# Kernel tuning notes

Hardware: AMD Instinct MI355X
Metric: run time of the kernel (lower is better)

## Reference

```python
import jax, jax.numpy as jnp
import numpy as np

LN_EPS = 1e-5

def _ln(x, g, b):
    # LayerNorm over last dim; torch normalized_shape=[1,H] on [B,1,H] reduces to this
    mu = jnp.mean(x, axis=-1, keepdims=True)
    var = jnp.var(x, axis=-1, keepdims=True)
    return (x - mu) * jax.lax.rsqrt(var + LN_EPS) * g + b


def setup_inputs() -> dict:
    key = jax.random.key(0)
    B, T, D, H = 32, 2048, 512, 128
    ks = jax.random.split(key, 10)
    stdu = 1.0 / np.sqrt(H)
    u = lambda k, sh: jax.random.uniform(k, sh, jnp.float32, -stdu, stdu)
    return {
        "x": jax.random.normal(ks[0], (B, T, D), jnp.float32),
        "W_f": u(ks[1], (D, H)), "W_i": u(ks[2], (D, H)),
        "W_o": u(ks[3], (D, H)), "W_c": u(ks[4], (D, H)),
        "U_f": u(ks[5], (H, H)), "U_i": u(ks[6], (H, H)),
        "U_o": u(ks[7], (H, H)), "U_c": u(ks[8], (H, H)),
        "b_f": jnp.ones((H,), jnp.float32),
        "b_i": jnp.zeros((H,), jnp.float32),
        "b_o": jnp.zeros((H,), jnp.float32),
        "b_c": jnp.zeros((H,), jnp.float32),
        "ln_f_g": jnp.ones((H,), jnp.float32), "ln_f_b": jnp.zeros((H,), jnp.float32),
        "ln_i_g": jnp.ones((H,), jnp.float32), "ln_i_b": jnp.zeros((H,), jnp.float32),
        "ln_o_g": jnp.ones((H,), jnp.float32), "ln_o_b": jnp.zeros((H,), jnp.float32),
        "ln_c_g": jnp.ones((H,), jnp.float32), "ln_c_b": jnp.zeros((H,), jnp.float32),
        "h0": jnp.zeros((B, H), jnp.float32),
        "c0": jnp.zeros((B, H), jnp.float32),
        "zoneout_mask": jax.random.randint(ks[9], (T,), 0, 2, jnp.int32),
    }


def reference(x, W_f, W_i, W_o, W_c, U_f, U_i, U_o, U_c,
              b_f, b_i, b_o, b_c,
              ln_f_g, ln_f_b, ln_i_g, ln_i_b, ln_o_g, ln_o_b, ln_c_g, ln_c_b,
              h0, c0, zoneout_mask):
    xs = jnp.swapaxes(x, 0, 1)                       # [T, B, D]
    m = zoneout_mask.astype(x.dtype)[:, None, None]  # [T, 1, 1] zoneout indicator

    def step(carry, inp):
        h, c = carry
        x_t, mt = inp
        f = jax.nn.sigmoid(_ln(x_t @ W_f + h @ U_f + b_f, ln_f_g, ln_f_b))
        i = jax.nn.sigmoid(_ln(x_t @ W_i + h @ U_i + b_i, ln_i_g, ln_i_b))
        o = jax.nn.sigmoid(_ln(x_t @ W_o + h @ U_o + b_o, ln_o_g, ln_o_b))
        ch = jax.nn.sigmoid(_ln(x_t @ W_c + h @ U_c + b_c, ln_c_g, ln_c_b))
        c_new = mt * c + (1.0 - mt) * (f * c + i * ch)
        # NOTE: source applies sigmoid (not tanh) to the cell state
        h_new = mt * h + (1.0 - mt) * (o * jax.nn.sigmoid(c_new))
        return (h_new, c_new), h_new

    (h_T, c_T), out_seq = jax.lax.scan(step, (h0, c0), (xs, m))
    return jnp.swapaxes(out_seq, 0, 1), h_T          # [B, T, H], [B, H]
```

## Files before the change

### kernel.cpp

```cpp
#include <hip/hip_runtime.h>
#include <hip/hip_bf16.h>

#define Bx 32
#define Tt 2048
#define Dd 512
#define Hh 128
#define PROW 520

typedef __attribute__((ext_vector_type(8))) short short8;
typedef __attribute__((ext_vector_type(4))) float f32x4;

static __device__ __forceinline__ short f2bf(float f) {
    __hip_bfloat16 h = __float2bfloat16(f);
    return *reinterpret_cast<short*>(&h);
}
static __device__ __forceinline__ float sigm(float x) {
    return 1.f / (1.f + __expf(-x));
}
static __device__ __forceinline__ float swz_xor16(float v) {
    return __int_as_float(__builtin_amdgcn_ds_swizzle(__float_as_int(v), 0x401F));
}

#define BARRIER_LGKM() asm volatile("s_waitcnt lgkmcnt(0)\n\ts_barrier" ::: "memory")

typedef __attribute__((address_space(1))) const void gas_void;
typedef __attribute__((address_space(3))) void las_void;
static __device__ __forceinline__ void gl_lds16(const float* g, float* l) {
    __builtin_amdgcn_global_load_lds((gas_void*)g, (las_void*)l, 16, 0, 0);
}

__global__ __launch_bounds__(512, 2) void gemm_xw_mfma(
    const float* __restrict__ X,
    const float* __restrict__ W0, const float* __restrict__ W1,
    const float* __restrict__ W2, const float* __restrict__ W3,
    const float* __restrict__ B0, const float* __restrict__ B1,
    const float* __restrict__ B2, const float* __restrict__ B3,
    float* __restrict__ G)
{
    __shared__ __align__(16) short As[128][40];
    __shared__ __align__(16) short Bs[512][40];

    const int tid  = threadIdx.x;
    const int m0   = blockIdx.x * 128;
    const int lane = tid & 63;
    const int w    = tid >> 6;
    const int wr   = w >> 2, wc = w & 3;
    const int l15  = lane & 15, kb = lane >> 4;

    const int bn   = tid;
    const int gate = bn >> 7;
    const int j    = bn & 127;
    const float* __restrict__ Wg = (gate == 0) ? W0 : (gate == 1) ? W1 : (gate == 2) ? W2 : W3;

    const int am = tid >> 2;
    const int ak = (tid & 3) * 8;

    const float* __restrict__ Bg = (wc == 0) ? B0 : (wc == 1) ? B1 : (wc == 2) ? B2 : B3;
    f32x4 acc[4][8];
    #pragma unroll
    for (int nt = 0; nt < 8; ++nt) {
        const float bv = Bg[nt * 16 + l15];
        #pragma unroll
        for (int mt = 0; mt < 4; ++mt)
            acc[mt][nt] = (f32x4){bv, bv, bv, bv};
    }

    for (int k0 = 0; k0 < Dd; k0 += 32) {
        {
            const float4* xp = (const float4*)&X[(size_t)(m0 + am) * Dd + k0 + ak];
            float4 v0 = xp[0], v1 = xp[1];
            short8 s;
            s[0] = f2bf(v0.x); s[1] = f2bf(v0.y); s[2] = f2bf(v0.z); s[3] = f2bf(v0.w);
            s[4] = f2bf(v1.x); s[5] = f2bf(v1.y); s[6] = f2bf(v1.z); s[7] = f2bf(v1.w);
            *(short8*)&As[am][ak] = s;
        }
        #pragma unroll
        for (int rc = 0; rc < 4; ++rc) {
            float v[8];
            #pragma unroll
            for (int r = 0; r < 8; ++r)
                v[r] = Wg[(size_t)(k0 + rc * 8 + r) * Hh + j];
            short8 s;
            #pragma unroll
            for (int r = 0; r < 8; ++r) s[r] = f2bf(v[r]);
            *(short8*)&Bs[bn][rc * 8] = s;
        }
        __syncthreads();

        short8 a[4], b[8];
        #pragma unroll
        for (int mt = 0; mt < 4; ++mt)
            a[mt] = *(const short8*)&As[wr * 64 + mt * 16 + l15][kb * 8];
        #pragma unroll
        for (int nt = 0; nt < 8; ++nt)
            b[nt] = *(const short8*)&Bs[wc * 128 + nt * 16 + l15][kb * 8];
        #pragma unroll
        for (int mt = 0; mt < 4; ++mt)
            #pragma unroll
            for (int nt = 0; nt < 8; ++nt)
                acc[mt][nt] = __builtin_amdgcn_mfma_f32_16x16x32_bf16(a[mt], b[nt], acc[mt][nt], 0, 0, 0);
        __syncthreads();
    }

    #pragma unroll
    for (int mt = 0; mt < 4; ++mt)
        #pragma unroll
        for (int nt = 0; nt < 8; ++nt)
            #pragma unroll
            for (int r = 0; r < 4; ++r)
                G[(size_t)(m0 + wr * 64 + mt * 16 + kb * 4 + r) * 512 + wc * 128 + nt * 16 + l15]
                    = acc[mt][nt][r];
}

__global__ __launch_bounds__(512, 1) void lstm_scan_mfma(
    const float* __restrict__ G,
    const float* __restrict__ Uf, const float* __restrict__ Ui,
    const float* __restrict__ Uo, const float* __restrict__ Uc,
    const float* __restrict__ lnfg, const float* __restrict__ lnfb,
    const float* __restrict__ lnig, const float* __restrict__ lnib,
    const float* __restrict__ lnog, const float* __restrict__ lnob,
    const float* __restrict__ lncg, const float* __restrict__ lncb,
    const float* __restrict__ h0, const float* __restrict__ c0,
    const int* __restrict__ zmask,
    float* __restrict__ out, float* __restrict__ hT)
{
    const int tid  = threadIdx.x;
    const int lane = tid & 63;
    const int w    = tid >> 6;
    const int b0   = blockIdx.x * 4;

    __shared__ __align__(16) short Ap[16 * 136];
    __shared__ __align__(16) float STb[4 * PROW];
    __shared__ __align__(16) float2 SQf[4][4][2][2];
    __shared__ __align__(16) float Pan[2 * 4 * 4 * PROW];
    __shared__ unsigned short act[Tt];
    __shared__ int wsum[8], wpre[8];
    __shared__ int nact_sh;

    const int gate = w >> 1;
    const float* __restrict__ Ug = (gate == 0) ? Uf : (gate == 1) ? Ui : (gate == 2) ? Uo : Uc;
    const int n0  = w * 64;
    const int l15 = lane & 15;
    const int kb  = lane >> 4;

    short8 bfr[4][4];
    #pragma unroll
    for (int nt = 0; nt < 4; ++nt) {
        const int jloc = (n0 & 127) + nt * 16 + l15;
        #pragma unroll
        for (int ks = 0; ks < 4; ++ks) {
            short8 v;
            #pragma unroll
            for (int r = 0; r < 8; ++r)
                v[r] = f2bf(Ug[(ks * 32 + kb * 8 + r) * Hh + jloc]);
            bfr[nt][ks] = v;
        }
    }

    const int ob = tid >> 7;
    const int oj = tid & 127;
    const float gamF = lnfg[oj], betF = lnfb[oj];
    const float gamI = lnig[oj], betI = lnib[oj];
    const float gamO = lnog[oj], betO = lnob[oj];
    const float gamC = lncg[oj], betC = lncb[oj];

    float hval = h0[(b0 + ob) * Hh + oj];
    float cval = c0[(b0 + ob) * Hh + oj];

    for (int i = tid; i < 16 * 136; i += 512) Ap[i] = 0;
    __syncthreads();
    Ap[ob * 136 + oj] = f2bf(hval);

    {
        const int base_t = tid * 4;
        const int f0 = (zmask[base_t] == 0), f1 = (zmask[base_t + 1] == 0);
        const int f2 = (zmask[base_t + 2] == 0), f3 = (zmask[base_t + 3] == 0);
        const int cnt = f0 + f1 + f2 + f3;
        int scan = cnt;
        #pragma unroll
        for (int off = 1; off <= 32; off <<= 1) {
            int v = __shfl_up(scan, off);
            if (lane >= off) scan += v;
        }
        if (lane == 63) wsum[w] = scan;
        __syncthreads();
        if (tid == 0) {
            int s = 0;
            #pragma unroll
            for (int i = 0; i < 8; ++i) { wpre[i] = s; s += wsum[i]; }
            nact_sh = s;
        }
        __syncthreads();
        int pos = wpre[w] + scan - cnt;
        if (f0) act[pos++] = (unsigned short)(base_t);
        if (f1) act[pos++] = (unsigned short)(base_t + 1);
        if (f2) act[pos++] = (unsigned short)(base_t + 2);
        if (f3) act[pos++] = (unsigned short)(base_t + 3);
    }
    __syncthreads();
    const int nact = nact_sh;

    auto stage_panel = [&](int kp, int buf) {
        #pragma unroll
        for (int si = 0; si < 2; ++si) {
            const int s    = w * 2 + si;
            const int slot = s >> 2;
            const int bb   = s & 3;
            const int kidx = kp + slot;
            if (kidx < nact) {
                const int tt = (int)act[kidx];
                const float* src = &G[((size_t)(b0 + bb) * Tt + tt) * 512];
                float* dst = &Pan[((buf * 4 + slot) * 4 + bb) * PROW];
                gl_lds16(src + lane * 4, dst);
                gl_lds16(src + 256 + lane * 4, dst + 256);
            }
        }
    };

    int cur = 0;
    stage_panel(0, 0);
    asm volatile("s_waitcnt vmcnt(0)" ::: "memory");
    __syncthreads();

    const int lb = l15 & 3;

    auto lstm_step = [&](int kidx, int slot) {
        const int t_ = (int)act[kidx];

        short8 a0 = *(const short8*)&Ap[l15 * 136 +  0 + kb * 8];
        short8 a1 = *(const short8*)&Ap[l15 * 136 + 32 + kb * 8];
        short8 a2 = *(const short8*)&Ap[l15 * 136 + 64 + kb * 8];
        short8 a3 = *(const short8*)&Ap[l15 * 136 + 96 + kb * 8];

        const int pbase = ((cur * 4 + slot) * 4 + lb) * PROW + n0 + kb * 4;
        f32x4 C0 = *(const f32x4*)&Pan[pbase];
        f32x4 C1 = *(const f32x4*)&Pan[pbase + 16];
        f32x4 C2 = *(const f32x4*)&Pan[pbase + 32];
        f32x4 C3 = *(const f32x4*)&Pan[pbase + 48];

        C0 = __builtin_amdgcn_mfma_f32_16x16x32_bf16(bfr[0][0], a0, C0, 0, 0, 0);
        C1 = __builtin_amdgcn_mfma_f32_16x16x32_bf16(bfr[1][0], a0, C1, 0, 0, 0);
        C2 = __builtin_amdgcn_mfma_f32_16x16x32_bf16(bfr[2][0], a0, C2, 0, 0, 0);
        C3 = __builtin_amdgcn_mfma_f32_16x16x32_bf16(bfr[3][0], a0, C3, 0, 0, 0);
        C0 = __builtin_amdgcn_mfma_f32_16x16x32_bf16(bfr[0][1], a1, C0, 0, 0, 0);
        C1 = __builtin_amdgcn_mfma_f32_16x16x32_bf16(bfr[1][1], a1, C1, 0, 0, 0);
        C2 = __builtin_amdgcn_mfma_f32_16x16x32_bf16(bfr[2][1], a1, C2, 0, 0, 0);
        C3 = __builtin_amdgcn_mfma_f32_16x16x32_bf16(bfr[3][1], a1, C3, 0, 0, 0);
        C0 = __builtin_amdgcn_mfma_f32_16x16x32_bf16(bfr[0][2], a2, C0, 0, 0, 0);
        C1 = __builtin_amdgcn_mfma_f32_16x16x32_bf16(bfr[1][2], a2, C1, 0, 0, 0);
        C2 = __builtin_amdgcn_mfma_f32_16x16x32_bf16(bfr[2][2], a2, C2, 0, 0, 0);
        C3 = __builtin_amdgcn_mfma_f32_16x16x32_bf16(bfr[3][2], a2, C3, 0, 0, 0);
        C0 = __builtin_amdgcn_mfma_f32_16x16x32_bf16(bfr[0][3], a3, C0, 0, 0, 0);
        C1 = __builtin_amdgcn_mfma_f32_16x16x32_bf16(bfr[1][3], a3, C1, 0, 0, 0);
        C2 = __builtin_amdgcn_mfma_f32_16x16x32_bf16(bfr[2][3], a3, C2, 0, 0, 0);
        C3 = __builtin_amdgcn_mfma_f32_16x16x32_bf16(bfr[3][3], a3, C3, 0, 0, 0);

        float ps = ((C0[0] + C0[1]) + (C0[2] + C0[3]))
                 + ((C1[0] + C1[1]) + (C1[2] + C1[3]))
                 + ((C2[0] + C2[1]) + (C2[2] + C2[3]))
                 + ((C3[0] + C3[1]) + (C3[2] + C3[3]));
        float pq = C0[0]*C0[0] + C0[1]*C0[1] + C0[2]*C0[2] + C0[3]*C0[3]
                 + C1[0]*C1[0] + C1[1]*C1[1] + C1[2]*C1[2] + C1[3]*C1[3]
                 + C2[0]*C2[0] + C2[1]*C2[1] + C2[2]*C2[2] + C2[3]*C2[3]
                 + C3[0]*C3[0] + C3[1]*C3[1] + C3[2]*C3[2] + C3[3]*C3[3];
        ps += swz_xor16(ps);
        pq += swz_xor16(pq);

        if (l15 < 4) {
            const int sbase = l15 * PROW + n0 + kb * 4;
            *(f32x4*)&STb[sbase]      = C0;
            *(f32x4*)&STb[sbase + 16] = C1;
            *(f32x4*)&STb[sbase + 32] = C2;
            *(f32x4*)&STb[sbase + 48] = C3;
            if ((kb & 1) == 0)
                SQf[gate][l15][w & 1][kb >> 1] = make_float2(ps, pq);
        }
        BARRIER_LGKM();

        const float sF = STb[ob * PROW +   0 + oj];
        const float sI = STb[ob * PROW + 128 + oj];
        const float sO = STb[ob * PROW + 256 + oj];
        const float sC = STb[ob * PROW + 384 + oj];
        f32x4 qF0 = *(const f32x4*)&SQf[0][ob][0][0];
        f32x4 qF1 = *(const f32x4*)&SQf[0][ob][1][0];
        f32x4 qI0 = *(const f32x4*)&SQf[1][ob][0][0];
        f32x4 qI1 = *(const f32x4*)&SQf[1][ob][1][0];
        f32x4 qO0 = *(const f32x4*)&SQf[2][ob][0][0];
        f32x4 qO1 = *(const f32x4*)&SQf[2][ob][1][0];
        f32x4 qC0 = *(const f32x4*)&SQf[3][ob][0][0];
        f32x4 qC1 = *(const f32x4*)&SQf[3][ob][1][0];
        const float SF = (qF0[0] + qF0[2]) + (qF1[0] + qF1[2]);
        const float QF = (qF0[1] + qF0[3]) + (qF1[1] + qF1[3]);
        const float SI = (qI0[0] + qI0[2]) + (qI1[0] + qI1[2]);
        const float QI = (qI0[1] + qI0[3]) + (qI1[1] + qI1[3]);
        const float SO = (qO0[0] + qO0[2]) + (qO1[0] + qO1[2]);
        const float QO = (qO0[1] + qO0[3]) + (qO1[1] + qO1[3]);
        const float SC = (qC0[0] + qC0[2]) + (qC1[0] + qC1[2]);
        const float QC = (qC0[1] + qC0[3]) + (qC1[1] + qC1[3]);
        const float muF = SF * (1.f/128.f), rF = rsqrtf(QF*(1.f/128.f) - muF*muF + 1e-5f);
        const float muI = SI * (1.f/128.f), rI = rsqrtf(QI*(1.f/128.f) - muI*muI + 1e-5f);
        const float muO = SO * (1.f/128.f), rO = rsqrtf(QO*(1.f/128.f) - muO*muO + 1e-5f);
        const float muC = SC * (1.f/128.f), rC = rsqrtf(QC*(1.f/128.f) - muC*muC + 1e-5f);
        const float gf  = sigm((sF - muF) * rF * gamF + betF);
        const float gi  = sigm((sI - muI) * rI * gamI + betI);
        const float go  = sigm((sO - muO) * rO * gamO + betO);
        const float gch = sigm((sC - muC) * rC * gamC + betC);
        cval = gf * cval + gi * gch;
        hval = go * sigm(cval);
        Ap[ob * 136 + oj] = f2bf(hval);
        out[((size_t)(b0 + ob) * Tt + t_) * Hh + oj] = hval;
    };

    for (int kp = 0; kp < nact; kp += 4) {
        stage_panel(kp + 4, cur ^ 1);
        const int lim = (nact - kp < 4) ? (nact - kp) : 4;
        #pragma unroll
        for (int sl = 0; sl < 4; ++sl) {
            if (sl < lim) {
                lstm_step(kp + sl, sl);
                if (sl == 3)
                    asm volatile("s_waitcnt vmcnt(0)" ::: "memory");
                BARRIER_LGKM();
            }
        }
        cur ^= 1;
    }

    hT[(b0 + ob) * Hh + oj] = hval;
}

__global__ __launch_bounds__(512) void fill_zoneout(
    const int* __restrict__ zmask, const float* __restrict__ h0,
    float* __restrict__ out)
{
    const int t = blockIdx.x;
    if (zmask[t] == 0) return;
    int s = t - 1;
    while (s >= 0 && zmask[s] != 0) --s;
    const int tid = threadIdx.x;
    for (int idx = tid; idx < Bx * Hh; idx += 512) {
        const int b = idx >> 7, j = idx & 127;
        const float v = (s >= 0) ? out[((size_t)b * Tt + s) * Hh + j]
                                 : h0[b * Hh + j];
        out[((size_t)b * Tt + t) * Hh + j] = v;
    }
}

extern "C" void kernel_launch(void* const* d_in, const int* in_sizes, int n_in,
                              void* d_out, int out_size, void* d_ws, size_t ws_size,
                              hipStream_t stream)
{
    const float* x   = (const float*)d_in[0];
    const float* W_f = (const float*)d_in[1];
    const float* W_i = (const float*)d_in[2];
    const float* W_o = (const float*)d_in[3];
    const float* W_c = (const float*)d_in[4];
    const float* U_f = (const float*)d_in[5];
    const float* U_i = (const float*)d_in[6];
    const float* U_o = (const float*)d_in[7];
    const float* U_c = (const float*)d_in[8];
    const float* b_f = (const float*)d_in[9];
    const float* b_i = (const float*)d_in[10];
    const float* b_o = (const float*)d_in[11];
    const float* b_c = (const float*)d_in[12];
    const float* ln_f_g = (const float*)d_in[13];
    const float* ln_f_b = (const float*)d_in[14];
    const float* ln_i_g = (const float*)d_in[15];
    const float* ln_i_b = (const float*)d_in[16];
    const float* ln_o_g = (const float*)d_in[17];
    const float* ln_o_b = (const float*)d_in[18];
    const float* ln_c_g = (const float*)d_in[19];
    const float* ln_c_b = (const float*)d_in[20];
    const float* h0  = (const float*)d_in[21];
    const float* c0  = (const float*)d_in[22];
    const int*   zm  = (const int*)d_in[23];

    float* out = (float*)d_out;
    float* hT  = out + (size_t)Bx * Tt * Hh;
    float* G   = (float*)d_ws;

    gemm_xw_mfma<<<(Bx * Tt) / 128, 512, 0, stream>>>(x, W_f, W_i, W_o, W_c,
                                                      b_f, b_i, b_o, b_c, G);

    lstm_scan_mfma<<<8, 512, 0, stream>>>(G, U_f, U_i, U_o, U_c,
                                          ln_f_g, ln_f_b, ln_i_g, ln_i_b,
                                          ln_o_g, ln_o_b, ln_c_g, ln_c_b,
                                          h0, c0, zm, out, hT);

    fill_zoneout<<<Tt, 512, 0, stream>>>(zm, h0, out);
}
```

Baseline: 1.738 ms.

## Remap scan waves to own all four gates per hidden slice, keeping activations in registers

Each wave now computes all four gate pre-activations for a 16-column slice of the hidden dimension, instead of one gate over 64 columns. The gate nonlinearity and cell update can then run directly on the MFMA accumulators in registers, with no round trip through a shared staging buffer. LayerNorm statistics are reduced through small partial-sum arrays and a single-wave DPP reduction, at the cost of an extra barrier per timestep. The elementwise stage now runs only in the 4-of-16 lanes that hold valid batch rows, so it uses fewer threads, but each does more work with vectorized stores.

Result: slower. 2.687 ms (+54.6%).

```diff
diff --git a/kernel.cpp b/kernel.cpp
--- a/kernel.cpp
+++ b/kernel.cpp
@@ -17,8 +17,10 @@
 static __device__ __forceinline__ float sigm(float x) {
     return 1.f / (1.f + __expf(-x));
 }
-static __device__ __forceinline__ float swz_xor16(float v) {
-    return __int_as_float(__builtin_amdgcn_ds_swizzle(__float_as_int(v), 0x401F));
+template<int CTRL>
+static __device__ __forceinline__ float dpp_add(float v) {
+    return v + __int_as_float(__builtin_amdgcn_update_dpp(
+        0, __float_as_int(v), CTRL, 0xF, 0xF, true));
 }
 
 #define BARRIER_LGKM() asm volatile("s_waitcnt lgkmcnt(0)\n\ts_barrier" ::: "memory")
@@ -129,47 +131,52 @@
     const int w    = tid >> 6;
     const int b0   = blockIdx.x * 4;
 
+    const int l15 = lane & 15;
+    const int kb  = lane >> 4;
+    const int lb  = l15 & 3;
+    const int j0  = w * 16;
+    const int jj  = j0 + kb * 4;
+
     __shared__ __align__(16) short Ap[16 * 136];
-    __shared__ __align__(16) float STb[4 * PROW];
-    __shared__ __align__(16) float2 SQf[4][4][2][2];
+    __shared__ __align__(16) float partPS[4 * 132];
+    __shared__ __align__(16) float partPQ[4 * 132];
+    __shared__ __align__(16) float2 stats[16];
     __shared__ __align__(16) float Pan[2 * 4 * 4 * PROW];
     __shared__ unsigned short act[Tt];
     __shared__ int wsum[8], wpre[8];
     __shared__ int nact_sh;
 
-    const int gate = w >> 1;
-    const float* __restrict__ Ug = (gate == 0) ? Uf : (gate == 1) ? Ui : (gate == 2) ? Uo : Uc;
-    const int n0  = w * 64;
-    const int l15 = lane & 15;
-    const int kb  = lane >> 4;
-
     short8 bfr[4][4];
     #pragma unroll
-    for (int nt = 0; nt < 4; ++nt) {
-        const int jloc = (n0 & 127) + nt * 16 + l15;
+    for (int g = 0; g < 4; ++g) {
+        const float* __restrict__ Ug = (g == 0) ? Uf : (g == 1) ? Ui : (g == 2) ? Uo : Uc;
         #pragma unroll
         for (int ks = 0; ks < 4; ++ks) {
             short8 v;
             #pragma unroll
             for (int r = 0; r < 8; ++r)
-                v[r] = f2bf(Ug[(ks * 32 + kb * 8 + r) * Hh + jloc]);
-            bfr[nt][ks] = v;
-        }
-    }
-
-    const int ob = tid >> 7;
-    const int oj = tid & 127;
-    const float gamF = lnfg[oj], betF = lnfb[oj];
-    const float gamI = lnig[oj], betI = lnib[oj];
-    const float gamO = lnog[oj], betO = lnob[oj];
-    const float gamC = lncg[oj], betC = lncb[oj];
-
-    float hval = h0[(b0 + ob) * Hh + oj];
-    float cval = c0[(b0 + ob) * Hh + oj];
+                v[r] = f2bf(Ug[(ks * 32 + kb * 8 + r) * Hh + j0 + l15]);
+            bfr[g][ks] = v;
+        }
+    }
+
+    f32x4 gam[4], bet[4];
+    gam[0] = *(const f32x4*)&lnfg[jj]; bet[0] = *(const f32x4*)&lnfb[jj];
+    gam[1] = *(const f32x4*)&lnig[jj]; bet[1] = *(const f32x4*)&lnib[jj];
+    gam[2] = *(const f32x4*)&lnog[jj]; bet[2] = *(const f32x4*)&lnob[jj];
+    gam[3] = *(const f32x4*)&lncg[jj]; bet[3] = *(const f32x4*)&lncb[jj];
+
+    f32x4 cv = *(const f32x4*)&c0[(b0 + lb) * Hh + jj];
+    f32x4 hv = *(const f32x4*)&h0[(b0 + lb) * Hh + jj];
 
     for (int i = tid; i < 16 * 136; i += 512) Ap[i] = 0;
     __syncthreads();
-    Ap[ob * 136 + oj] = f2bf(hval);
+    if (l15 < 4) {
+        short hp[4];
+        #pragma unroll
+        for (int r = 0; r < 4; ++r) hp[r] = f2bf(hv[r]);
+        *(short4*)&Ap[l15 * 136 + jj] = *(short4*)hp;
+    }
 
     {
         const int base_t = tid * 4;
@@ -222,8 +229,6 @@
     asm volatile("s_waitcnt vmcnt(0)" ::: "memory");
     __syncthreads();
 
-    const int lb = l15 & 3;
-
     auto lstm_step = [&](int kidx, int slot) {
         const int t_ = (int)act[kidx];
 
@@ -232,11 +237,11 @@
         short8 a2 = *(const short8*)&Ap[l15 * 136 + 64 + kb * 8];
         short8 a3 = *(const short8*)&Ap[l15 * 136 + 96 + kb * 8];
 
-        const int pbase = ((cur * 4 + slot) * 4 + lb) * PROW + n0 + kb * 4;
-        f32x4 C0 = *(const f32x4*)&Pan[pbase];
-        f32x4 C1 = *(const f32x4*)&Pan[pbase + 16];
-        f32x4 C2 = *(const f32x4*)&Pan[pbase + 32];
-        f32x4 C3 = *(const f32x4*)&Pan[pbase + 48];
+        const int pbase = ((cur * 4 + slot) * 4 + lb) * PROW;
+        f32x4 C0 = *(const f32x4*)&Pan[pbase +   0 + jj];
+        f32x4 C1 = *(const f32x4*)&Pan[pbase + 128 + jj];
+        f32x4 C2 = *(const f32x4*)&Pan[pbase + 256 + jj];
+        f32x4 C3 = *(const f32x4*)&Pan[pbase + 384 + jj];
 
         C0 = __builtin_amdgcn_mfma_f32_16x16x32_bf16(bfr[0][0], a0, C0, 0, 0, 0);
         C1 = __builtin_amdgcn_mfma_f32_16x16x32_bf16(bfr[1][0], a0, C1, 0, 0, 0);
@@ -255,60 +260,64 @@
         C2 = __builtin_amdgcn_mfma_f32_16x16x32_bf16(bfr[2][3], a3, C2, 0, 0, 0);
         C3 = __builtin_amdgcn_mfma_f32_16x16x32_bf16(bfr[3][3], a3, C3, 0, 0, 0);
 
-        float ps = ((C0[0] + C0[1]) + (C0[2] + C0[3]))
-                 + ((C1[0] + C1[1]) + (C1[2] + C1[3]))
-                 + ((C2[0] + C2[1]) + (C2[2] + C2[3]))
-                 + ((C3[0] + C3[1]) + (C3[2] + C3[3]));
-        float pq = C0[0]*C0[0] + C0[1]*C0[1] + C0[2]*C0[2] + C0[3]*C0[3]
-                 + C1[0]*C1[0] + C1[1]*C1[1] + C1[2]*C1[2] + C1[3]*C1[3]
-                 + C2[0]*C2[0] + C2[1]*C2[1] + C2[2]*C2[2] + C2[3]*C2[3]
-                 + C3[0]*C3[0] + C3[1]*C3[1] + C3[2]*C3[2] + C3[3]*C3[3];
-        ps += swz_xor16(ps);
-        pq += swz_xor16(pq);
-
+        f32x4 psv, pqv;
+        psv[0] = (C0[0] + C0[1]) + (C0[2] + C0[3]);
+        psv[1] = (C1[0] + C1[1]) + (C1[2] + C1[3]);
+        psv[2] = (C2[0] + C2[1]) + (C2[2] + C2[3]);
+        psv[3] = (C3[0] + C3[1]) + (C3[2] + C3[3]);
+        pqv[0] = C0[0]*C0[0] + C0[1]*C0[1] + C0[2]*C0[2] + C0[3]*C0[3];
+        pqv[1] = C1[0]*C1[0] + C1[1]*C1[1] + C1[2]*C1[2] + C1[3]*C1[3];
+        pqv[2] = C2[0]*C2[0] + C2[1]*C2[1] + C2[2]*C2[2] + C2[3]*C2[3];
+        pqv[3] = C3[0]*C3[0] + C3[1]*C3[1] + C3[2]*C3[2] + C3[3]*C3[3];
         if (l15 < 4) {
-            const int sbase = l15 * PROW + n0 + kb * 4;
-            *(f32x4*)&STb[sbase]      = C0;
-            *(f32x4*)&STb[sbase + 16] = C1;
-            *(f32x4*)&STb[sbase + 32] = C2;
-            *(f32x4*)&STb[sbase + 48] = C3;
-            if ((kb & 1) == 0)
-                SQf[gate][l15][w & 1][kb >> 1] = make_float2(ps, pq);
+            const int pa = l15 * 132 + (w * 4 + kb) * 4;
+            *(f32x4*)&partPS[pa] = psv;
+            *(f32x4*)&partPQ[pa] = pqv;
         }
         BARRIER_LGKM();
 
-        const float sF = STb[ob * PROW +   0 + oj];
-        const float sI = STb[ob * PROW + 128 + oj];
-        const float sO = STb[ob * PROW + 256 + oj];
-        const float sC = STb[ob * PROW + 384 + oj];
-        f32x4 qF0 = *(const f32x4*)&SQf[0][ob][0][0];
-        f32x4 qF1 = *(const f32x4*)&SQf[0][ob][1][0];
-        f32x4 qI0 = *(const f32x4*)&SQf[1][ob][0][0];
-        f32x4 qI1 = *(const f32x4*)&SQf[1][ob][1][0];
-        f32x4 qO0 = *(const f32x4*)&SQf[2][ob][0][0];
-        f32x4 qO1 = *(const f32x4*)&SQf[2][ob][1][0];
-        f32x4 qC0 = *(const f32x4*)&SQf[3][ob][0][0];
-        f32x4 qC1 = *(const f32x4*)&SQf[3][ob][1][0];
-        const float SF = (qF0[0] + qF0[2]) + (qF1[0] + qF1[2]);
-        const float QF = (qF0[1] + qF0[3]) + (qF1[1] + qF1[3]);
-        const float SI = (qI0[0] + qI0[2]) + (qI1[0] + qI1[2]);
-        const float QI = (qI0[1] + qI0[3]) + (qI1[1] + qI1[3]);
-        const float SO = (qO0[0] + qO0[2]) + (qO1[0] + qO1[2]);
-        const float QO = (qO0[1] + qO0[3]) + (qO1[1] + qO1[3]);
-        const float SC = (qC0[0] + qC0[2]) + (qC1[0] + qC1[2]);
-        const float QC = (qC0[1] + qC0[3]) + (qC1[1] + qC1[3]);
-        const float muF = SF * (1.f/128.f), rF = rsqrtf(QF*(1.f/128.f) - muF*muF + 1e-5f);
-        const float muI = SI * (1.f/128.f), rI = rsqrtf(QI*(1.f/128.f) - muI*muI + 1e-5f);
-        const float muO = SO * (1.f/128.f), rO = rsqrtf(QO*(1.f/128.f) - muO*muO + 1e-5f);
-        const float muC = SC * (1.f/128.f), rC = rsqrtf(QC*(1.f/128.f) - muC*muC + 1e-5f);
-        const float gf  = sigm((sF - muF) * rF * gamF + betF);
-        const float gi  = sigm((sI - muI) * rI * gamI + betI);
-        const float go  = sigm((sO - muO) * rO * gamO + betO);
-        const float gch = sigm((sC - muC) * rC * gamC + betC);
-        cval = gf * cval + gi * gch;
-        hval = go * sigm(cval);
-        Ap[ob * 136 + oj] = f2bf(hval);
-        out[((size_t)(b0 + ob) * Tt + t_) * Hh + oj] = hval;
+        if (w == 0) {
+            const int bg = lane >> 2;
+            const int bq = bg >> 2, gq = bg & 3;
+            const int ch = lane & 3;
+            float S = 0.f, Q = 0.f;
+            #pragma unroll
+            for (int i = 0; i < 8; ++i) {
+                const int pa = bq * 132 + (ch * 8 + i) * 4 + gq;
+                S += partPS[pa];
+                Q += partPQ[pa];
+            }
+            S = dpp_add<0xB1>(S); S = dpp_add<0x4E>(S);
+            Q = dpp_add<0xB1>(Q); Q = dpp_add<0x4E>(Q);
+            if (ch == 0) stats[bg] = make_float2(S, Q);
+        }
+        BARRIER_LGKM();
+
+        if (l15 < 4) {
+            f32x4 st01 = *(const f32x4*)&stats[l15 * 4];
+            f32x4 st23 = *(const f32x4*)&stats[l15 * 4 + 2];
+            const float mu0 = st01[0] * (1.f/128.f), r0 = rsqrtf(st01[1]*(1.f/128.f) - mu0*mu0 + 1e-5f);
+            const float mu1 = st01[2] * (1.f/128.f), r1 = rsqrtf(st01[3]*(1.f/128.f) - mu1*mu1 + 1e-5f);
+            const float mu2 = st23[0] * (1.f/128.f), r2 = rsqrtf(st23[1]*(1.f/128.f) - mu2*mu2 + 1e-5f);
+            const float mu3 = st23[2] * (1.f/128.f), r3 = rsqrtf(st23[3]*(1.f/128.f) - mu3*mu3 + 1e-5f);
+            f32x4 hnew;
+            #pragma unroll
+            for (int r = 0; r < 4; ++r) {
+                const float gf  = sigm((C0[r] - mu0) * r0 * gam[0][r] + bet[0][r]);
+                const float gi  = sigm((C1[r] - mu1) * r1 * gam[1][r] + bet[1][r]);
+                const float go  = sigm((C2[r] - mu2) * r2 * gam[2][r] + bet[2][r]);
+                const float gch = sigm((C3[r] - mu3) * r3 * gam[3][r] + bet[3][r]);
+                cv[r] = gf * cv[r] + gi * gch;
+                hnew[r] = go * sigm(cv[r]);
+            }
+            hv = hnew;
+            short hp[4];
+            #pragma unroll
+            for (int r = 0; r < 4; ++r) hp[r] = f2bf(hv[r]);
+            *(short4*)&Ap[l15 * 136 + jj] = *(short4*)hp;
+            float4 ho = make_float4(hv[0], hv[1], hv[2], hv[3]);
+            *(float4*)&out[((size_t)(b0 + l15) * Tt + t_) * Hh + jj] = ho;
+        }
     };
 
     for (int kp = 0; kp < nact; kp += 4) {
@@ -326,7 +335,10 @@
         cur ^= 1;
     }
 
-    hT[(b0 + ob) * Hh + oj] = hval;
+    if (l15 < 4) {
+        float4 ho = make_float4(hv[0], hv[1], hv[2], hv[3]);
+        *(float4*)&hT[(b0 + l15) * Hh + jj] = ho;
+    }
 }
 
 __global__ __launch_bounds__(512) void fill_zoneout(
```

## Assign one wave per gate in LSTM scan to keep LayerNorm stats in-wave

Applied to the files above, without the earlier changes.

The recurrent scan kernel drops from 8 waves to 4, and each wave now computes the full 128-wide pre-activation for one gate. LayerNorm mean and variance are therefore reduced entirely within the wave using a swizzle plus a shuffle, and each wave normalises its own values before writing them to shared memory. This removes the cross-wave exchange of partial statistics and simplifies the gate epilogue. In exchange, each wave issues twice as many serial MFMAs per timestep, each thread handles two hidden units, and every step still needs two barriers. The kernel also now writes h0 into the output for timesteps before the first active one.

Result: faster. 1.614 ms (-7.1%).

```diff
diff --git a/kernel.cpp b/kernel.cpp
--- a/kernel.cpp
+++ b/kernel.cpp
@@ -5,7 +5,9 @@
 #define Tt 2048
 #define Dd 512
 #define Hh 128
+#define APS 152
 #define PROW 520
+#define SGS 528
 
 typedef __attribute__((ext_vector_type(8))) short short8;
 typedef __attribute__((ext_vector_type(4))) float f32x4;
@@ -17,8 +19,8 @@
 static __device__ __forceinline__ float sigm(float x) {
     return 1.f / (1.f + __expf(-x));
 }
-static __device__ __forceinline__ float swz_xor16(float v) {
-    return __int_as_float(__builtin_amdgcn_ds_swizzle(__float_as_int(v), 0x401F));
+static __device__ __forceinline__ float swz_xor16_add(float v) {
+    return v + __int_as_float(__builtin_amdgcn_ds_swizzle(__float_as_int(v), 0x401F));
 }
 
 #define BARRIER_LGKM() asm volatile("s_waitcnt lgkmcnt(0)\n\ts_barrier" ::: "memory")
@@ -112,7 +114,7 @@
                     = acc[mt][nt][r];
 }
 
-__global__ __launch_bounds__(512, 1) void lstm_scan_mfma(
+__global__ __launch_bounds__(256, 1) void lstm_scan_mfma(
     const float* __restrict__ G,
     const float* __restrict__ Uf, const float* __restrict__ Ui,
     const float* __restrict__ Uo, const float* __restrict__ Uc,
@@ -128,54 +130,51 @@
     const int lane = tid & 63;
     const int w    = tid >> 6;
     const int b0   = blockIdx.x * 4;
-
-    __shared__ __align__(16) short Ap[16 * 136];
-    __shared__ __align__(16) float STb[4 * PROW];
-    __shared__ __align__(16) float2 SQf[4][4][2][2];
+    const int l15  = lane & 15;
+    const int kb   = lane >> 4;
+
+    __shared__ __align__(16) short Ap[16 * APS];
+    __shared__ __align__(16) float SLN[4 * SGS];
     __shared__ __align__(16) float Pan[2 * 4 * 4 * PROW];
     __shared__ unsigned short act[Tt];
-    __shared__ int wsum[8], wpre[8];
+    __shared__ int wsum[4], wpre[4];
     __shared__ int nact_sh;
 
-    const int gate = w >> 1;
-    const float* __restrict__ Ug = (gate == 0) ? Uf : (gate == 1) ? Ui : (gate == 2) ? Uo : Uc;
-    const int n0  = w * 64;
-    const int l15 = lane & 15;
-    const int kb  = lane >> 4;
-
-    short8 bfr[4][4];
+    const float* __restrict__ Ug = (w == 0) ? Uf : (w == 1) ? Ui : (w == 2) ? Uo : Uc;
+    short8 bfr[8][4];
     #pragma unroll
-    for (int nt = 0; nt < 4; ++nt) {
-        const int jloc = (n0 & 127) + nt * 16 + l15;
+    for (int nt = 0; nt < 8; ++nt) {
         #pragma unroll
         for (int ks = 0; ks < 4; ++ks) {
             short8 v;
             #pragma unroll
             for (int r = 0; r < 8; ++r)
-                v[r] = f2bf(Ug[(ks * 32 + kb * 8 + r) * Hh + jloc]);
+                v[r] = f2bf(Ug[(ks * 32 + kb * 8 + r) * Hh + nt * 16 + l15]);
             bfr[nt][ks] = v;
         }
     }
 
-    const int ob = tid >> 7;
-    const int oj = tid & 127;
-    const float gamF = lnfg[oj], betF = lnfb[oj];
-    const float gamI = lnig[oj], betI = lnib[oj];
-    const float gamO = lnog[oj], betO = lnob[oj];
-    const float gamC = lncg[oj], betC = lncb[oj];
-
-    float hval = h0[(b0 + ob) * Hh + oj];
-    float cval = c0[(b0 + ob) * Hh + oj];
-
-    for (int i = tid; i < 16 * 136; i += 512) Ap[i] = 0;
+    const int j1 = lane, j2 = lane + 64;
+    const float gF1 = lnfg[j1], bF1 = lnfb[j1], gF2 = lnfg[j2], bF2 = lnfb[j2];
+    const float gI1 = lnig[j1], bI1 = lnib[j1], gI2 = lnig[j2], bI2 = lnib[j2];
+    const float gO1 = lnog[j1], bO1 = lnob[j1], gO2 = lnog[j2], bO2 = lnob[j2];
+    const float gC1 = lncg[j1], bC1 = lncb[j1], gC2 = lncg[j2], bC2 = lncb[j2];
+
+    float hv0 = h0[(b0 + w) * Hh + j1];
+    float hv1 = h0[(b0 + w) * Hh + j2];
+    float cv0 = c0[(b0 + w) * Hh + j1];
+    float cv1 = c0[(b0 + w) * Hh + j2];
+
+    for (int i = tid; i < 16 * APS; i += 256) Ap[i] = 0;
     __syncthreads();
-    Ap[ob * 136 + oj] = f2bf(hval);
+    Ap[w * APS + j1] = f2bf(hv0);
+    Ap[w * APS + j2] = f2bf(hv1);
 
     {
-        const int base_t = tid * 4;
-        const int f0 = (zmask[base_t] == 0), f1 = (zmask[base_t + 1] == 0);
-        const int f2 = (zmask[base_t + 2] == 0), f3 = (zmask[base_t + 3] == 0);
-        const int cnt = f0 + f1 + f2 + f3;
+        const int base_t = tid * 8;
+        int fl[8], cnt = 0;
+        #pragma unroll
+        for (int i = 0; i < 8; ++i) { fl[i] = (zmask[base_t + i] == 0); cnt += fl[i]; }
         int scan = cnt;
         #pragma unroll
         for (int off = 1; off <= 32; off <<= 1) {
@@ -187,23 +186,28 @@
         if (tid == 0) {
             int s = 0;
             #pragma unroll
-            for (int i = 0; i < 8; ++i) { wpre[i] = s; s += wsum[i]; }
+            for (int i = 0; i < 4; ++i) { wpre[i] = s; s += wsum[i]; }
             nact_sh = s;
         }
         __syncthreads();
         int pos = wpre[w] + scan - cnt;
-        if (f0) act[pos++] = (unsigned short)(base_t);
-        if (f1) act[pos++] = (unsigned short)(base_t + 1);
-        if (f2) act[pos++] = (unsigned short)(base_t + 2);
-        if (f3) act[pos++] = (unsigned short)(base_t + 3);
+        #pragma unroll
+        for (int i = 0; i < 8; ++i)
+            if (fl[i]) act[pos++] = (unsigned short)(base_t + i);
     }
     __syncthreads();
     const int nact = nact_sh;
 
+    const int firstA = (nact > 0) ? (int)act[0] : Tt;
+    for (int tt = 0; tt < firstA; ++tt) {
+        out[((size_t)(b0 + w) * Tt + tt) * Hh + j1] = hv0;
+        out[((size_t)(b0 + w) * Tt + tt) * Hh + j2] = hv1;
+    }
+
     auto stage_panel = [&](int kp, int buf) {
         #pragma unroll
-        for (int si = 0; si < 2; ++si) {
-            const int s    = w * 2 + si;
+        for (int si = 0; si < 4; ++si) {
+            const int s    = w * 4 + si;
             const int slot = s >> 2;
             const int bb   = s & 3;
             const int kidx = kp + slot;
@@ -227,88 +231,82 @@
     auto lstm_step = [&](int kidx, int slot) {
         const int t_ = (int)act[kidx];
 
-        short8 a0 = *(const short8*)&Ap[l15 * 136 +  0 + kb * 8];
-        short8 a1 = *(const short8*)&Ap[l15 * 136 + 32 + kb * 8];
-        short8 a2 = *(const short8*)&Ap[l15 * 136 + 64 + kb * 8];
-        short8 a3 = *(const short8*)&Ap[l15 * 136 + 96 + kb * 8];
-
-        const int pbase = ((cur * 4 + slot) * 4 + lb) * PROW + n0 + kb * 4;
-        f32x4 C0 = *(const f32x4*)&Pan[pbase];
-        f32x4 C1 = *(const f32x4*)&Pan[pbase + 16];
-        f32x4 C2 = *(const f32x4*)&Pan[pbase + 32];
-        f32x4 C3 = *(const f32x4*)&Pan[pbase + 48];
-
-        C0 = __builtin_amdgcn_mfma_f32_16x16x32_bf16(bfr[0][0], a0, C0, 0, 0, 0);
-        C1 = __builtin_amdgcn_mfma_f32_16x16x32_bf16(bfr[1][0], a0, C1, 0, 0, 0);
-        C2 = __builtin_amdgcn_mfma_f32_16x16x32_bf16(bfr[2][0], a0, C2, 0, 0, 0);
-        C3 = __builtin_amdgcn_mfma_f32_16x16x32_bf16(bfr[3][0], a0, C3, 0, 0, 0);
-        C0 = __builtin_amdgcn_mfma_f32_16x16x32_bf16(bfr[0][1], a1, C0, 0, 0, 0);
-        C1 = __builtin_amdgcn_mfma_f32_16x16x32_bf16(bfr[1][1], a1, C1, 0, 0, 0);
-        C2 = __builtin_amdgcn_mfma_f32_16x16x32_bf16(bfr[2][1], a1, C2, 0, 0, 0);
-        C3 = __builtin_amdgcn_mfma_f32_16x16x32_bf16(bfr[3][1], a1, C3, 0, 0, 0);
-        C0 = __builtin_amdgcn_mfma_f32_16x16x32_bf16(bfr[0][2], a2, C0, 0, 0, 0);
-        C1 = __builtin_amdgcn_mfma_f32_16x16x32_bf16(bfr[1][2], a2, C1, 0, 0, 0);
-        C2 = __builtin_amdgcn_mfma_f32_16x16x32_bf16(bfr[2][2], a2, C2, 0, 0, 0);
-        C3 = __builtin_amdgcn_mfma_f32_16x16x32_bf16(bfr[3][2], a2, C3, 0, 0, 0);
-        C0 = __builtin_amdgcn_mfma_f32_16x16x32_bf16(bfr[0][3], a3, C0, 0, 0, 0);
-        C1 = __builtin_amdgcn_mfma_f32_16x16x32_bf16(bfr[1][3], a3, C1, 0, 0, 0);
-        C2 = __builtin_amdgcn_mfma_f32_16x16x32_bf16(bfr[2][3], a3, C2, 0, 0, 0);
-        C3 = __builtin_amdgcn_mfma_f32_16x16x32_bf16(bfr[3][3], a3, C3, 0, 0, 0);
-
-        float ps = ((C0[0] + C0[1]) + (C0[2] + C0[3]))
-                 + ((C1[0] + C1[1]) + (C1[2] + C1[3]))
-                 + ((C2[0] + C2[1]) + (C2[2] + C2[3]))
-                 + ((C3[0] + C3[1]) + (C3[2] + C3[3]));
-        float pq = C0[0]*C0[0] + C0[1]*C0[1] + C0[2]*C0[2] + C0[3]*C0[3]
-                 + C1[0]*C1[0] + C1[1]*C1[1] + C1[2]*C1[2] + C1[3]*C1[3]
-                 + C2[0]*C2[0] + C2[1]*C2[1] + C2[2]*C2[2] + C2[3]*C2[3]
-                 + C3[0]*C3[0] + C3[1]*C3[1] + C3[2]*C3[2] + C3[3]*C3[3];
-        ps += swz_xor16(ps);
-        pq += swz_xor16(pq);
+        short8 a0 = *(const short8*)&Ap[l15 * APS +  0 + kb * 8];
+        short8 a1 = *(const short8*)&Ap[l15 * APS + 32 + kb * 8];
+        short8 a2 = *(const short8*)&Ap[l15 * APS + 64 + kb * 8];
+        short8 a3 = *(const short8*)&Ap[l15 * APS + 96 + kb * 8];
+
+        const int pbase = ((cur * 4 + slot) * 4 + lb) * PROW + w * 128 + kb * 4;
+        f32x4 Cv[8];
+        #pragma unroll
+        for (int nt = 0; nt < 8; ++nt)
+            Cv[nt] = *(const f32x4*)&Pan[pbase + nt * 16];
+
+        #pragma unroll
+        for (int nt = 0; nt < 8; ++nt)
+            Cv[nt] = __builtin_amdgcn_mfma_f32_16x16x32_bf16(bfr[nt][0], a0, Cv[nt], 0, 0, 0);
+        #pragma unroll
+        for (int nt = 0; nt < 8; ++nt)
+            Cv[nt] = __builtin_amdgcn_mfma_f32_16x16x32_bf16(bfr[nt][1], a1, Cv[nt], 0, 0, 0);
+        #pragma unroll
+        for (int nt = 0; nt < 8; ++nt)
+            Cv[nt] = __builtin_amdgcn_mfma_f32_16x16x32_bf16(bfr[nt][2], a2, Cv[nt], 0, 0, 0);
+        #pragma unroll
+        for (int nt = 0; nt < 8; ++nt)
+            Cv[nt] = __builtin_amdgcn_mfma_f32_16x16x32_bf16(bfr[nt][3], a3, Cv[nt], 0, 0, 0);
+
+        float sm = 0.f, sq = 0.f;
+        #pragma unroll
+        for (int nt = 0; nt < 8; ++nt)
+            #pragma unroll
+            for (int r = 0; r < 4; ++r) {
+                sm += Cv[nt][r];
+                sq = fmaf(Cv[nt][r], Cv[nt][r], sq);
+            }
+        sm = swz_xor16_add(sm);
+        sq = swz_xor16_add(sq);
+        sm += __shfl_xor(sm, 32);
+        sq += __shfl_xor(sq, 32);
+        const float mu   = sm * (1.f / 128.f);
+        const float rstd = rsqrtf(sq * (1.f / 128.f) - mu * mu + 1e-5f);
+        const float na = rstd, nc = -mu * rstd;
+        #pragma unroll
+        for (int nt = 0; nt < 8; ++nt)
+            #pragma unroll
+            for (int r = 0; r < 4; ++r)
+                Cv[nt][r] = fmaf(Cv[nt][r], na, nc);
 
         if (l15 < 4) {
-            const int sbase = l15 * PROW + n0 + kb * 4;
-            *(f32x4*)&STb[sbase]      = C0;
-            *(f32x4*)&STb[sbase + 16] = C1;
-            *(f32x4*)&STb[sbase + 32] = C2;
-            *(f32x4*)&STb[sbase + 48] = C3;
-            if ((kb & 1) == 0)
-                SQf[gate][l15][w & 1][kb >> 1] = make_float2(ps, pq);
+            #pragma unroll
+            for (int nt = 0; nt < 8; ++nt)
+                *(f32x4*)&SLN[w * SGS + l15 * 132 + nt * 16 + kb * 4] = Cv[nt];
         }
         BARRIER_LGKM();
 
-        const float sF = STb[ob * PROW +   0 + oj];
-        const float sI = STb[ob * PROW + 128 + oj];
-        const float sO = STb[ob * PROW + 256 + oj];
-        const float sC = STb[ob * PROW + 384 + oj];
-        f32x4 qF0 = *(const f32x4*)&SQf[0][ob][0][0];
-        f32x4 qF1 = *(const f32x4*)&SQf[0][ob][1][0];
-        f32x4 qI0 = *(const f32x4*)&SQf[1][ob][0][0];
-        f32x4 qI1 = *(const f32x4*)&SQf[1][ob][1][0];
-        f32x4 qO0 = *(const f32x4*)&SQf[2][ob][0][0];
-        f32x4 qO1 = *(const f32x4*)&SQf[2][ob][1][0];
-        f32x4 qC0 = *(const f32x4*)&SQf[3][ob][0][0];
-        f32x4 qC1 = *(const f32x4*)&SQf[3][ob][1][0];
-        const float SF = (qF0[0] + qF0[2]) + (qF1[0] + qF1[2]);
-        const float QF = (qF0[1] + qF0[3]) + (qF1[1] + qF1[3]);
-        const float SI = (qI0[0] + qI0[2]) + (qI1[0] + qI1[2]);
-        const float QI = (qI0[1] + qI0[3]) + (qI1[1] + qI1[3]);
-        const float SO = (qO0[0] + qO0[2]) + (qO1[0] + qO1[2]);
-        const float QO = (qO0[1] + qO0[3]) + (qO1[1] + qO1[3]);
-        const float SC = (qC0[0] + qC0[2]) + (qC1[0] + qC1[2]);
-        const float QC = (qC0[1] + qC0[3]) + (qC1[1] + qC1[3]);
-        const float muF = SF * (1.f/128.f), rF = rsqrtf(QF*(1.f/128.f) - muF*muF + 1e-5f);
-        const float muI = SI * (1.f/128.f), rI = rsqrtf(QI*(1.f/128.f) - muI*muI + 1e-5f);
-        const float muO = SO * (1.f/128.f), rO = rsqrtf(QO*(1.f/128.f) - muO*muO + 1e-5f);
-        const float muC = SC * (1.f/128.f), rC = rsqrtf(QC*(1.f/128.f) - muC*muC + 1e-5f);
-        const float gf  = sigm((sF - muF) * rF * gamF + betF);
-        const float gi  = sigm((sI - muI) * rI * gamI + betI);
-        const float go  = sigm((sO - muO) * rO * gamO + betO);
-        const float gch = sigm((sC - muC) * rC * gamC + betC);
-        cval = gf * cval + gi * gch;
-        hval = go * sigm(cval);
-        Ap[ob * 136 + oj] = f2bf(hval);
-        out[((size_t)(b0 + ob) * Tt + t_) * Hh + oj] = hval;
+        {
+            const int sb = w * 132;
+            const float nf0 = SLN[0 * SGS + sb + j1], nf1 = SLN[0 * SGS + sb + j2];
+            const float ni0 = SLN[1 * SGS + sb + j1], ni1 = SLN[1 * SGS + sb + j2];
+            const float no0 = SLN[2 * SGS + sb + j1], no1 = SLN[2 * SGS + sb + j2];
+            const float nc0 = SLN[3 * SGS + sb + j1], nc1 = SLN[3 * SGS + sb + j2];
+            const float f0 = sigm(fmaf(nf0, gF1, bF1));
+            const float i0 = sigm(fmaf(ni0, gI1, bI1));
+            const float o0 = sigm(fmaf(no0, gO1, bO1));
+            const float g0 = sigm(fmaf(nc0, gC1, bC1));
+            const float f1 = sigm(fmaf(nf1, gF2, bF2));
+            const float i1 = sigm(fmaf(ni1, gI2, bI2));
+            const float o1 = sigm(fmaf(no1, gO2, bO2));
+            const float g1 = sigm(fmaf(nc1, gC2, bC2));
+            cv0 = f0 * cv0 + i0 * g0;
+            hv0 = o0 * sigm(cv0);
+            cv1 = f1 * cv1 + i1 * g1;
+            hv1 = o1 * sigm(cv1);
+            Ap[w * APS + j1] = f2bf(hv0);
+            Ap[w * APS + j2] = f2bf(hv1);
+            out[((size_t)(b0 + w) * Tt + t_) * Hh + j1] = hv0;
+            out[((size_t)(b0 + w) * Tt + t_) * Hh + j2] = hv1;
+        }
+        BARRIER_LGKM();
     };
 
     for (int kp = 0; kp < nact; kp += 4) {
@@ -320,13 +318,13 @@
                 lstm_step(kp + sl, sl);
                 if (sl == 3)
                     asm volatile("s_waitcnt vmcnt(0)" ::: "memory");
-                BARRIER_LGKM();
             }
         }
         cur ^= 1;
     }
 
-    hT[(b0 + ob) * Hh + oj] = hval;
+    hT[(b0 + w) * Hh + j1] = hv0;
+    hT[(b0 + w) * Hh + j2] = hv1;
 }
 
 __global__ __launch_bounds__(512) void fill_zoneout(
@@ -382,7 +380,7 @@
     gemm_xw_mfma<<<(Bx * Tt) / 128, 512, 0, stream>>>(x, W_f, W_i, W_o, W_c,
                                                       b_f, b_i, b_o, b_c, G);
 
-    lstm_scan_mfma<<<8, 512, 0, stream>>>(G, U_f, U_i, U_o, U_c,
+    lstm_scan_mfma<<<8, 256, 0, stream>>>(G, U_f, U_i, U_o, U_c,
                                           ln_f_g, ln_f_b, ln_i_g, ln_i_b,
                                           ln_o_g, ln_o_b, ln_c_g, ln_c_b,
                                           h0, c0, zm, out, hT);
```
